# Kernel optimization log

Measured on AMD Instinct MI355X. Metric: run time of the kernel, lower is better.

Reference implementation:

```python
import jax, jax.numpy as jnp
import numpy as np

B, N, DIM, H, DH, MLP, L = 4, 1024, 1024, 16, 64, 4096, 2
C = DIM // 4  # conditioning dim = 256


def setup_inputs() -> dict:
    key = jax.random.key(0)
    ks = jax.random.split(key, 12)
    s = 0.02
    return dict(
        x=jax.random.normal(ks[0], (B, N, DIM), jnp.float32),
        mu=jax.random.normal(ks[1], (B, N, C), jnp.float32),
        f=jax.random.normal(ks[2], (B, N, C), jnp.float32),
        Wqkv=jax.random.normal(ks[3], (L, DIM, 3 * H * DH), jnp.float32) * s,
        Wout=jax.random.normal(ks[4], (L, H * DH, DIM), jnp.float32) * s,
        bout=jnp.zeros((L, DIM), jnp.float32),
        W1=jax.random.normal(ks[5], (L, DIM, MLP), jnp.float32) * s,
        b1=jnp.zeros((L, MLP), jnp.float32),
        W2=jax.random.normal(ks[6], (L, MLP, DIM), jnp.float32) * s,
        b2=jnp.zeros((L, DIM), jnp.float32),
        Wmu=jax.random.normal(ks[7], (L, C, 6 * C), jnp.float32) * s,
        bmu=jnp.zeros((L, 6 * C), jnp.float32),
        Wf=jax.random.normal(ks[8], (L, C, 6 * 3 * C), jnp.float32) * s,
        bf=jnp.zeros((L, 6 * 3 * C), jnp.float32),
        g1=jnp.ones((L, DIM), jnp.float32),
        be1=jnp.zeros((L, DIM), jnp.float32),
        g2=jnp.ones((L, DIM), jnp.float32),
        be2=jnp.zeros((L, DIM), jnp.float32),
    )


def _ln(x, g, b):
    m = jnp.mean(x, -1, keepdims=True)
    v = jnp.mean((x - m) ** 2, -1, keepdims=True)
    return (x - m) * jax.lax.rsqrt(v + 1e-5) * g + b


def reference(x, mu, f, Wqkv, Wout, bout, W1, b1, W2, b2, Wmu, bmu, Wf, bf, g1, be1, g2, be2):
    scale = DH ** -0.5
    smu = jax.nn.silu(mu)  # SiLU applied to raw conditioning, shared across layers
    sf = jax.nn.silu(f)
    for i in range(L):
        mm = smu @ Wmu[i] + bmu[i]          # [B,N,6*C]
        mf = sf @ Wf[i] + bf[i]             # [B,N,6*3*C]
        mus = jnp.split(mm, 6, axis=-1)     # each [B,N,C]
        fs = jnp.split(mf, 6, axis=-1)      # each [B,N,3C]
        sh_a, sc_a, ga_a, sh_m, sc_m, ga_m = [
            jnp.concatenate([a, b_], -1) for a, b_ in zip(mus, fs)
        ]                                   # each [B,N,DIM]
        # attention branch
        h = _ln(x, g1[i], be1[i]) * (1 + sc_a) + sh_a
        qkv = h @ Wqkv[i]                   # [B,N,3*H*DH]
        q, k, v = [t.reshape(B, N, H, DH) for t in jnp.split(qkv, 3, axis=-1)]
        att = jax.nn.softmax(jnp.einsum('bihd,bjhd->bhij', q, k) * scale, axis=-1)
        o = jnp.einsum('bhij,bjhd->bihd', att, v).reshape(B, N, H * DH)
        x = x + ga_a * (o @ Wout[i] + bout[i])
        # MLP branch
        h2 = _ln(x, g2[i], be2[i]) * (1 + sc_m) + sh_m
        mlp = jax.nn.gelu(h2 @ W1[i] + b1[i], approximate=False) @ W2[i] + b2[i]
        x = x + ga_m * mlp
    return x
```

## Files before the change

### kernel.cpp

```cpp
#include <hip/hip_runtime.h>
#include <math.h>

#define BB 4
#define NN 1024
#define DIMD 1024
#define HHN 16
#define DHH 64
#define MLPD 4096
#define LLN 2
#define CCD 256
#define BNROWS (BB*NN)

typedef __attribute__((ext_vector_type(8))) _Float16 h8;
typedef __attribute__((ext_vector_type(4))) _Float16 h4;
typedef __attribute__((ext_vector_type(4))) float f32x4;

#define GLD16(gp, lp) __builtin_amdgcn_global_load_lds( \
    (const __attribute__((address_space(1))) void*)(gp), \
    (__attribute__((address_space(3))) void*)(lp), 16, 0, 0)

__global__ __launch_bounds__(256) void silu_kernel(const float* __restrict__ in,
                                                   _Float16* __restrict__ out, int n4) {
  int i = blockIdx.x * 256 + threadIdx.x;
  if (i < n4) {
    float4 v = ((const float4*)in)[i];
    h4 o;
    o[0] = (_Float16)(v.x / (1.f + __expf(-v.x)));
    o[1] = (_Float16)(v.y / (1.f + __expf(-v.y)));
    o[2] = (_Float16)(v.z / (1.f + __expf(-v.z)));
    o[3] = (_Float16)(v.w / (1.f + __expf(-v.w)));
    ((h4*)out)[i] = o;
  }
}

__global__ __launch_bounds__(256) void transpose_cast(const float* __restrict__ in,
                                                      _Float16* __restrict__ out,
                                                      int K, int N) {
  __shared__ float tile[64][68];
  int bx = blockIdx.x * 64;
  int by = blockIdx.y * 64;
  int tid = threadIdx.x;
  int r0 = tid >> 4, c4 = (tid & 15) * 4;
  #pragma unroll
  for (int i = 0; i < 4; i++) {
    float4 v = *(const float4*)(in + (size_t)(by + r0 + i * 16) * N + bx + c4);
    *(float4*)&tile[r0 + i * 16][c4] = v;
  }
  __syncthreads();
  #pragma unroll
  for (int i = 0; i < 4; i++) {
    int orow = r0 + i * 16;
    h4 o;
    #pragma unroll
    for (int j = 0; j < 4; j++) o[j] = (_Float16)tile[c4 + j][orow];
    *(h4*)(out + (size_t)(bx + orow) * K + by + c4) = o;
  }
}

__global__ __launch_bounds__(256) void v_transpose(const _Float16* __restrict__ qkv,
                                                   _Float16* __restrict__ vt) {
  __shared__ _Float16 t[64][72];
  int n0 = blockIdx.x * 64;
  int bh = blockIdx.y;
  int b = bh >> 4;
  const _Float16* src = qkv + (size_t)b * NN * 3072 + 2048 + (bh & 15) * 64;
  int tid = threadIdx.x;
  int row = tid >> 2, c0 = (tid & 3) * 16;
  *(h8*)&t[row][c0] = *(const h8*)(src + (size_t)(n0 + row) * 3072 + c0);
  *(h8*)&t[row][c0 + 8] = *(const h8*)(src + (size_t)(n0 + row) * 3072 + c0 + 8);
  __syncthreads();
  int d = tid >> 2, ns = (tid & 3) * 16;
  h8 o0, o1;
  #pragma unroll
  for (int j = 0; j < 8; j++) { o0[j] = t[ns + j][d]; o1[j] = t[ns + 8 + j][d]; }
  _Float16* dst = vt + ((size_t)bh * 64 + d) * NN + n0 + ns;
  *(h8*)dst = o0;
  *(h8*)(dst + 8) = o1;
}

template <int EPI, int BNT>
__global__ __launch_bounds__(256) void gemm_bt(
    const _Float16* __restrict__ A, const _Float16* __restrict__ Bt,
    int M, int Nt, int K,
    const float* __restrict__ bias,
    _Float16* __restrict__ outh) {
  constexpr int NREP = BNT / 32;
  __shared__ _Float16 As[3][128 * 32];
  __shared__ _Float16 Bs[3][BNT * 32];
  const int tid = threadIdx.x;
  const int wave = tid >> 6, lane = tid & 63;
  const int brow = blockIdx.x * 128, bcol = blockIdx.y * BNT;
  const int wr = (wave >> 1) * 64, wc = (wave & 1) * (BNT / 2);
  const int r = lane & 15, g = lane >> 4;
  f32x4 acc[4][NREP];
  #pragma unroll
  for (int m = 0; m < 4; m++)
    #pragma unroll
    for (int n = 0; n < NREP; n++) acc[m][n] = (f32x4){0.f, 0.f, 0.f, 0.f};

  const int scol = ((lane & 3) ^ ((lane >> 3) & 3)) * 8;
  const _Float16* gA = A + (size_t)(brow + wave * 32 + (lane >> 2)) * K + scol;
  const _Float16* gB = Bt + (size_t)(bcol + wave * (BNT / 4) + (lane >> 2)) * K + scol;

  auto STAGE = [&](int slot, int k0) {
    GLD16(gA + k0, &As[slot][wave * 1024]);
    GLD16(gA + k0 + 16 * (size_t)K, &As[slot][wave * 1024 + 512]);
    if (BNT == 128) {
      GLD16(gB + k0, &Bs[slot][wave * 1024]);
      GLD16(gB + k0 + 16 * (size_t)K, &Bs[slot][wave * 1024 + 512]);
    } else {
      GLD16(gB + k0, &Bs[slot][wave * 512]);
    }
  };

  const int NT = K / 32;
  #pragma unroll
  for (int s = 0; s < 3; ++s)
    if (s < NT) STAGE(s, s * 32);

  const int gg = g ^ ((r >> 1) & 3);

  int cur = 0;
  for (int t = 0; t < NT; ++t) {
    const int rem = NT - 1 - t;
    if constexpr (BNT == 128) {
      if (rem >= 2)      asm volatile("s_waitcnt vmcnt(8)" ::: "memory");
      else if (rem == 1) asm volatile("s_waitcnt vmcnt(4)" ::: "memory");
      else               asm volatile("s_waitcnt vmcnt(0)" ::: "memory");
    } else {
      if (rem >= 2)      asm volatile("s_waitcnt vmcnt(6)" ::: "memory");
      else if (rem == 1) asm volatile("s_waitcnt vmcnt(3)" ::: "memory");
      else               asm volatile("s_waitcnt vmcnt(0)" ::: "memory");
    }
    __builtin_amdgcn_s_barrier();
    h8 af[4], bfr[NREP];
    #pragma unroll
    for (int m = 0; m < 4; m++) af[m] = *(const h8*)(&As[cur][(wr + m * 16 + r) * 32 + gg * 8]);
    #pragma unroll
    for (int n = 0; n < NREP; n++) bfr[n] = *(const h8*)(&Bs[cur][(wc + n * 16 + r) * 32 + gg * 8]);
    #pragma unroll
    for (int m = 0; m < 4; m++)
      #pragma unroll
      for (int n = 0; n < NREP; n++)
        acc[m][n] = __builtin_amdgcn_mfma_f32_16x16x32_f16(bfr[n], af[m], acc[m][n], 0, 0, 0);
    asm volatile("s_waitcnt lgkmcnt(0)" ::: "memory");
    __builtin_amdgcn_s_barrier();
    if (t + 3 < NT) STAGE(cur, (t + 3) * 32);
    cur = (cur == 2) ? 0 : cur + 1;
  }

  #pragma unroll
  for (int m = 0; m < 4; m++) {
    const int grow = brow + wr + m * 16 + r;
    #pragma unroll
    for (int n = 0; n < NREP; n++) {
      const int gcol = bcol + wc + n * 16 + 4 * g;
      float4 bv4 = bias ? *(const float4*)(bias + gcol) : float4{0.f, 0.f, 0.f, 0.f};
      float v[4] = {acc[m][n][0] + bv4.x, acc[m][n][1] + bv4.y,
                    acc[m][n][2] + bv4.z, acc[m][n][3] + bv4.w};
      h4 o;
      if (EPI == 0) {
        #pragma unroll
        for (int q = 0; q < 4; q++) o[q] = (_Float16)v[q];
      } else {
        #pragma unroll
        for (int q = 0; q < 4; q++)
          o[q] = (_Float16)(0.5f * v[q] * (1.f + erff(v[q] * 0.70710678118f)));
      }
      *(h4*)(outh + (size_t)grow * Nt + gcol) = o;
    }
  }
}

__global__ __launch_bounds__(256) void ln_mod_res(
    float* __restrict__ x,
    const _Float16* __restrict__ delta,
    const _Float16* __restrict__ mga, const _Float16* __restrict__ fga, int jga,
    const _Float16* __restrict__ msc, const _Float16* __restrict__ fsc, int jsh, int jsc,
    const float* __restrict__ gam, const float* __restrict__ bet,
    _Float16* __restrict__ hout) {
  const int row = blockIdx.x;
  const int tid = threadIdx.x;
  const int c0 = tid * 4;
  float* xr = x + (size_t)row * DIMD;
  float4 v = *(float4*)(xr + c0);
  if (delta) {
    h4 d4 = *(const h4*)(delta + (size_t)row * DIMD + c0);
    h4 g4 = (c0 < CCD)
        ? *(const h4*)(mga + (size_t)row * (6 * CCD) + jga * CCD + c0)
        : *(const h4*)(fga + (size_t)row * (18 * CCD) + jga * (3 * CCD) + (c0 - CCD));
    v.x += (float)g4[0] * (float)d4[0];
    v.y += (float)g4[1] * (float)d4[1];
    v.z += (float)g4[2] * (float)d4[2];
    v.w += (float)g4[3] * (float)d4[3];
    *(float4*)(xr + c0) = v;
  }
  float s = v.x + v.y + v.z + v.w;
  float sq = v.x * v.x + v.y * v.y + v.z * v.z + v.w * v.w;
  #pragma unroll
  for (int off = 32; off > 0; off >>= 1) {
    s += __shfl_down(s, off);
    sq += __shfl_down(sq, off);
  }
  __shared__ float red[8];
  int wv = tid >> 6, ln = tid & 63;
  if (ln == 0) { red[wv] = s; red[4 + wv] = sq; }
  __syncthreads();
  s = red[0] + red[1] + red[2] + red[3];
  sq = red[4] + red[5] + red[6] + red[7];
  float mean = s * (1.f / DIMD);
  float var = sq * (1.f / DIMD) - mean * mean;
  float rs = rsqrtf(var + 1e-5f);
  float4 gm = *(const float4*)(gam + c0);
  float4 bt = *(const float4*)(bet + c0);
  h4 sh4 = (c0 < CCD)
      ? *(const h4*)(msc + (size_t)row * (6 * CCD) + jsh * CCD + c0)
      : *(const h4*)(fsc + (size_t)row * (18 * CCD) + jsh * (3 * CCD) + (c0 - CCD));
  h4 sc4 = (c0 < CCD)
      ? *(const h4*)(msc + (size_t)row * (6 * CCD) + jsc * CCD + c0)
      : *(const h4*)(fsc + (size_t)row * (18 * CCD) + jsc * (3 * CCD) + (c0 - CCD));
  float xv[4] = {v.x, v.y, v.z, v.w};
  float gv[4] = {gm.x, gm.y, gm.z, gm.w};
  float bv[4] = {bt.x, bt.y, bt.z, bt.w};
  h4 o;
  #pragma unroll
  for (int i = 0; i < 4; i++) {
    float lnv = (xv[i] - mean) * rs * gv[i] + bv[i];
    o[i] = (_Float16)(lnv * (1.f + (float)sc4[i]) + (float)sh4[i]);
  }
  *((h4*)(hout + (size_t)row * DIMD + c0)) = o;
}

__global__ __launch_bounds__(256) void res_final(
    float* __restrict__ x, const _Float16* __restrict__ delta,
    const _Float16* __restrict__ mga, const _Float16* __restrict__ fga, int jga) {
  const int row = blockIdx.x;
  const int c0 = threadIdx.x * 4;
  float* xr = x + (size_t)row * DIMD;
  float4 v = *(float4*)(xr + c0);
  h4 d4 = *(const h4*)(delta + (size_t)row * DIMD + c0);
  h4 g4 = (c0 < CCD)
      ? *(const h4*)(mga + (size_t)row * (6 * CCD) + jga * CCD + c0)
      : *(const h4*)(fga + (size_t)row * (18 * CCD) + jga * (3 * CCD) + (c0 - CCD));
  v.x += (float)g4[0] * (float)d4[0];
  v.y += (float)g4[1] * (float)d4[1];
  v.z += (float)g4[2] * (float)d4[2];
  v.w += (float)g4[3] * (float)d4[3];
  *(float4*)(xr + c0) = v;
}

__global__ __launch_bounds__(256) void attn_kernel(const _Float16* __restrict__ qkv,
                                                   const _Float16* __restrict__ vt,
                                                   _Float16* __restrict__ o) {
  __shared__ _Float16 Ks[2 * 64 * 64];
  __shared__ _Float16 Vs[2 * 64 * 64];
  __shared__ _Float16 Ps[4][32 * 72];
  const int bhg = blockIdx.x * 8 + (blockIdx.y & 7);
  const int qt = blockIdx.y >> 3;
  const int b = bhg >> 4, hh = bhg & 15;
  const int tid = threadIdx.x;
  const int wave = tid >> 6, lane = tid & 63;
  const int r = lane & 15, g = lane >> 4;
  const int RS = 3 * HHN * DHH;
  const _Float16* qb = qkv + (size_t)b * NN * RS + hh * DHH;
  const _Float16* kb = qb + HHN * DHH;
  const _Float16* vtb = vt + (size_t)bhg * DHH * NN;
  const int q0 = qt * 128 + wave * 32;

  h8 qf[2][2];
  #pragma unroll
  for (int m = 0; m < 2; m++) {
    qf[m][0] = *(const h8*)(qb + (size_t)(q0 + m * 16 + r) * RS + g * 8);
    qf[m][1] = *(const h8*)(qb + (size_t)(q0 + m * 16 + r) * RS + 32 + g * 8);
  }

  f32x4 oacc[2][4];
  #pragma unroll
  for (int m = 0; m < 2; m++)
    #pragma unroll
    for (int n = 0; n < 4; n++) oacc[m][n] = (f32x4){0.f, 0.f, 0.f, 0.f};
  float mrun[2][4], lrun[2][4];
  #pragma unroll
  for (int m = 0; m < 2; m++)
    #pragma unroll
    for (int q = 0; q < 4; q++) { mrun[m][q] = -1e30f; lrun[m][q] = 0.f; }
  const float scale = 0.125f;
  _Float16* Pw = Ps[wave];

  auto STAGE = [&](int buf, int k0) {
    #pragma unroll
    for (int i = 0; i < 2; i++) {
      int chunk = wave * 2 + i;
      int blk = chunk * 64 + lane;
      int row = blk >> 3, c16 = blk & 7;
      int sc = ((c16 ^ (row & 7))) * 8;
      GLD16(kb + (size_t)(k0 + row) * RS + sc, Ks + buf * 4096 + chunk * 512);
      GLD16(vtb + (size_t)row * NN + k0 + sc, Vs + buf * 4096 + chunk * 512);
    }
  };

  STAGE(0, 0);
  int cur = 0;
  for (int kt = 0; kt < NN / 64; ++kt) {
    __syncthreads();
    if (kt + 1 < NN / 64) STAGE(cur ^ 1, (kt + 1) * 64);
    const _Float16* Kb = Ks + cur * 4096;
    const _Float16* Vb = Vs + cur * 4096;
    f32x4 sfr[2][4];
    #pragma unroll
    for (int m = 0; m < 2; m++)
      #pragma unroll
      for (int n = 0; n < 4; n++) sfr[m][n] = (f32x4){0.f, 0.f, 0.f, 0.f};
    #pragma unroll
    for (int n = 0; n < 4; n++) {
      int row = n * 16 + r, sw = row & 7;
      h8 kf0 = *(const h8*)(Kb + row * 64 + (g ^ sw) * 8);
      h8 kf1 = *(const h8*)(Kb + row * 64 + ((4 + g) ^ sw) * 8);
      #pragma unroll
      for (int m = 0; m < 2; m++) {
        sfr[m][n] = __builtin_amdgcn_mfma_f32_16x16x32_f16(qf[m][0], kf0, sfr[m][n], 0, 0, 0);
        sfr[m][n] = __builtin_amdgcn_mfma_f32_16x16x32_f16(qf[m][1], kf1, sfr[m][n], 0, 0, 0);
      }
    }
    #pragma unroll
    for (int m = 0; m < 2; m++) {
      float pm[4];
      #pragma unroll
      for (int q = 0; q < 4; q++)
        pm[q] = fmaxf(fmaxf(sfr[m][0][q], sfr[m][1][q]), fmaxf(sfr[m][2][q], sfr[m][3][q])) * scale;
      #pragma unroll
      for (int off = 1; off < 16; off <<= 1)
        #pragma unroll
        for (int q = 0; q < 4; q++) pm[q] = fmaxf(pm[q], __shfl_xor(pm[q], off));
      float fac[4], rsum[4];
      #pragma unroll
      for (int q = 0; q < 4; q++) {
        float mn = fmaxf(mrun[m][q], pm[q]);
        fac[q] = __expf(mrun[m][q] - mn);
        mrun[m][q] = mn;
        rsum[q] = 0.f;
      }
      #pragma unroll
      for (int n = 0; n < 4; n++)
        #pragma unroll
        for (int q = 0; q < 4; q++) {
          float p = __expf(sfr[m][n][q] * scale - mrun[m][q]);
          sfr[m][n][q] = p;
          rsum[q] += p;
        }
      #pragma unroll
      for (int off = 1; off < 16; off <<= 1)
        #pragma unroll
        for (int q = 0; q < 4; q++) rsum[q] += __shfl_xor(rsum[q], off);
      #pragma unroll
      for (int q = 0; q < 4; q++) lrun[m][q] = lrun[m][q] * fac[q] + rsum[q];
      #pragma unroll
      for (int n = 0; n < 4; n++)
        #pragma unroll
        for (int q = 0; q < 4; q++) oacc[m][n][q] *= fac[q];
      #pragma unroll
      for (int n = 0; n < 4; n++)
        #pragma unroll
        for (int q = 0; q < 4; q++)
          Pw[(m * 16 + 4 * g + q) * 72 + n * 16 + r] = (_Float16)sfr[m][n][q];
    }
    h8 pa[2][2];
    #pragma unroll
    for (int m = 0; m < 2; m++) {
      pa[m][0] = *(const h8*)(Pw + (m * 16 + r) * 72 + g * 8);
      pa[m][1] = *(const h8*)(Pw + (m * 16 + r) * 72 + 32 + g * 8);
    }
    #pragma unroll
    for (int nd = 0; nd < 4; nd++) {
      int row = nd * 16 + r, sw = row & 7;
      h8 vf0 = *(const h8*)(Vb + row * 64 + (g ^ sw) * 8);
      h8 vf1 = *(const h8*)(Vb + row * 64 + ((4 + g) ^ sw) * 8);
      #pragma unroll
      for (int m = 0; m < 2; m++) {
        oacc[m][nd] = __builtin_amdgcn_mfma_f32_16x16x32_f16(pa[m][0], vf0, oacc[m][nd], 0, 0, 0);
        oacc[m][nd] = __builtin_amdgcn_mfma_f32_16x16x32_f16(pa[m][1], vf1, oacc[m][nd], 0, 0, 0);
      }
    }
    cur ^= 1;
  }
  #pragma unroll
  for (int m = 0; m < 2; m++)
    #pragma unroll
    for (int nd = 0; nd < 4; nd++)
      #pragma unroll
      for (int q = 0; q < 4; q++) {
        int row = q0 + m * 16 + 4 * g + q;
        int col = hh * DHH + nd * 16 + r;
        o[((size_t)b * NN + row) * DIMD + col] = (_Float16)(oacc[m][nd][q] / lrun[m][q]);
      }
}

extern "C" void kernel_launch(void* const* d_in, const int* in_sizes, int n_in,
                              void* d_out, int out_size, void* d_ws, size_t ws_size,
                              hipStream_t stream) {
  (void)in_sizes; (void)n_in; (void)out_size; (void)ws_size;
  const float* mu   = (const float*)d_in[1];
  const float* f_in = (const float*)d_in[2];
  const float* Wqkv = (const float*)d_in[3];
  const float* Wout = (const float*)d_in[4];
  const float* bout = (const float*)d_in[5];
  const float* W1   = (const float*)d_in[6];
  const float* b1   = (const float*)d_in[7];
  const float* W2   = (const float*)d_in[8];
  const float* b2   = (const float*)d_in[9];
  const float* Wmu  = (const float*)d_in[10];
  const float* bmu  = (const float*)d_in[11];
  const float* Wf   = (const float*)d_in[12];
  const float* bfv  = (const float*)d_in[13];
  const float* g1   = (const float*)d_in[14];
  const float* be1  = (const float*)d_in[15];
  const float* g2   = (const float*)d_in[16];
  const float* be2  = (const float*)d_in[17];
  float* xout = (float*)d_out;

  char* ws = (char*)d_ws;
  size_t off = 0;
  auto alloc = [&](size_t elems) -> _Float16* {
    _Float16* p = (_Float16*)(ws + off);
    off += ((elems * 2 + 255) / 256) * 256;
    return p;
  };
  _Float16* wTqkv = alloc((size_t)LLN * 3072 * 1024);
  _Float16* wTout = alloc((size_t)LLN * 1024 * 1024);
  _Float16* wT1   = alloc((size_t)LLN * 4096 * 1024);
  _Float16* wT2   = alloc((size_t)LLN * 1024 * 4096);
  _Float16* wTmu  = alloc((size_t)LLN * 1536 * 256);
  _Float16* wTf   = alloc((size_t)LLN * 4608 * 256);
  _Float16* smu   = alloc((size_t)BNROWS * CCD);
  _Float16* sfb   = alloc((size_t)BNROWS * CCD);
  _Float16* mmb[2] = {alloc((size_t)BNROWS * 6 * CCD), alloc((size_t)BNROWS * 6 * CCD)};
  _Float16* mfb[2] = {alloc((size_t)BNROWS * 18 * CCD), alloc((size_t)BNROWS * 18 * CCD)};
  _Float16* hbuf  = alloc((size_t)BNROWS * DIMD);
  _Float16* qkvb  = alloc((size_t)BNROWS * 3 * DIMD);
  _Float16* obuf  = alloc((size_t)BNROWS * DIMD);
  _Float16* m1b   = alloc((size_t)BNROWS * MLPD);
  _Float16* vtb   = alloc((size_t)BNROWS * DIMD);
  _Float16* dres  = alloc((size_t)BNROWS * DIMD);

  hipMemcpyAsync(d_out, d_in[0], (size_t)BNROWS * DIMD * sizeof(float),
                 hipMemcpyDeviceToDevice, stream);

  silu_kernel<<<BNROWS * CCD / 4 / 256, 256, 0, stream>>>(mu, smu, BNROWS * CCD / 4);
  silu_kernel<<<BNROWS * CCD / 4 / 256, 256, 0, stream>>>(f_in, sfb, BNROWS * CCD / 4);

  for (int l = 0; l < LLN; l++) {
    transpose_cast<<<dim3(3072 / 64, 1024 / 64), 256, 0, stream>>>(
        Wqkv + (size_t)l * 1024 * 3072, wTqkv + (size_t)l * 3072 * 1024, 1024, 3072);
    transpose_cast<<<dim3(1024 / 64, 1024 / 64), 256, 0, stream>>>(
        Wout + (size_t)l * 1024 * 1024, wTout + (size_t)l * 1024 * 1024, 1024, 1024);
    transpose_cast<<<dim3(4096 / 64, 1024 / 64), 256, 0, stream>>>(
        W1 + (size_t)l * 1024 * 4096, wT1 + (size_t)l * 4096 * 1024, 1024, 4096);
    transpose_cast<<<dim3(1024 / 64, 4096 / 64), 256, 0, stream>>>(
        W2 + (size_t)l * 4096 * 1024, wT2 + (size_t)l * 1024 * 4096, 4096, 1024);
    transpose_cast<<<dim3(1536 / 64, 256 / 64), 256, 0, stream>>>(
        Wmu + (size_t)l * 256 * 1536, wTmu + (size_t)l * 1536 * 256, 256, 1536);
    transpose_cast<<<dim3(4608 / 64, 256 / 64), 256, 0, stream>>>(
        Wf + (size_t)l * 256 * 4608, wTf + (size_t)l * 4608 * 256, 256, 4608);
  }

  for (int l = 0; l < LLN; l++) {
    gemm_bt<0, 64><<<dim3(BNROWS / 128, 1536 / 64), 256, 0, stream>>>(
        smu, wTmu + (size_t)l * 1536 * 256, BNROWS, 1536, 256,
        bmu + (size_t)l * 1536, mmb[l]);
    gemm_bt<0, 128><<<dim3(BNROWS / 128, 4608 / 128), 256, 0, stream>>>(
        sfb, wTf + (size_t)l * 4608 * 256, BNROWS, 4608, 256,
        bfv + (size_t)l * 4608, mfb[l]);
    ln_mod_res<<<BNROWS, 256, 0, stream>>>(
        xout, (l == 0) ? nullptr : dres,
        mmb[l ^ 1], mfb[l ^ 1], 5,
        mmb[l], mfb[l], 0, 1,
        g1 + (size_t)l * DIMD, be1 + (size_t)l * DIMD, hbuf);
    gemm_bt<0, 128><<<dim3(BNROWS / 128, 3072 / 128), 256, 0, stream>>>(
        hbuf, wTqkv + (size_t)l * 3072 * 1024, BNROWS, 3072, 1024,
        nullptr, qkvb);
    v_transpose<<<dim3(NN / 64, BB * HHN), 256, 0, stream>>>(qkvb, vtb);
    attn_kernel<<<dim3(NN / 128, BB * HHN), 256, 0, stream>>>(qkvb, vtb, obuf);
    gemm_bt<0, 64><<<dim3(BNROWS / 128, 1024 / 64), 256, 0, stream>>>(
        obuf, wTout + (size_t)l * 1024 * 1024, BNROWS, 1024, 1024,
        bout + (size_t)l * DIMD, dres);
    ln_mod_res<<<BNROWS, 256, 0, stream>>>(
        xout, dres,
        mmb[l], mfb[l], 2,
        mmb[l], mfb[l], 3, 4,
        g2 + (size_t)l * DIMD, be2 + (size_t)l * DIMD, hbuf);
    gemm_bt<1, 128><<<dim3(BNROWS / 128, 4096 / 128), 256, 0, stream>>>(
        hbuf, wT1 + (size_t)l * 4096 * 1024, BNROWS, 4096, 1024,
        b1 + (size_t)l * MLPD, m1b);
    gemm_bt<0, 64><<<dim3(BNROWS / 128, 1024 / 64), 256, 0, stream>>>(
        m1b, wT2 + (size_t)l * 1024 * 4096, BNROWS, 1024, 4096,
        b2 + (size_t)l * DIMD, dres);
  }
  res_final<<<BNROWS, 256, 0, stream>>>(xout, dres, mmb[(LLN - 1) & 1], mfb[(LLN - 1) & 1], 5);
}
```

Before: 724.1 us.

## Split-K the N=1024 GEMMs and reduce partials in LayerNorm residual kernels

The out-projection and W2 GEMMs, which have only 1024 output columns, now use a 4-way split-K over a third grid dimension. Each split writes an fp16 partial buffer, and the downstream residual/LayerNorm kernels sum the partials and add the bias, so the grid has more blocks to fill the GPU. All GEMMs now share a 128x128 tile with a simpler double-buffered __syncthreads pipeline, replacing the triple-buffered vmcnt pipeline. The cost is extra partial-buffer traffic, fp16 rounding of each partial, and possibly weaker load/compute overlap in the large GEMMs.

```diff
diff --git a/kernel.cpp b/kernel.cpp
--- a/kernel.cpp
+++ b/kernel.cpp
@@ -10,6 +10,7 @@
 #define LLN 2
 #define CCD 256
 #define BNROWS (BB*NN)
+#define NSPLIT 4
 
 typedef __attribute__((ext_vector_type(8))) _Float16 h8;
 typedef __attribute__((ext_vector_type(4))) _Float16 h4;
@@ -78,103 +79,86 @@
   *(h8*)(dst + 8) = o1;
 }
 
-template <int EPI, int BNT>
-__global__ __launch_bounds__(256) void gemm_bt(
+template <int EPI>
+__global__ __launch_bounds__(256) void gemm128(
     const _Float16* __restrict__ A, const _Float16* __restrict__ Bt,
-    int M, int Nt, int K,
-    const float* __restrict__ bias,
-    _Float16* __restrict__ outh) {
-  constexpr int NREP = BNT / 32;
-  __shared__ _Float16 As[3][128 * 32];
-  __shared__ _Float16 Bs[3][BNT * 32];
+    int M, int Nt, int Ktot, int Kper,
+    const float* __restrict__ bias, _Float16* __restrict__ outp) {
+  __shared__ _Float16 As[2][128 * 32];
+  __shared__ _Float16 Bs[2][128 * 32];
   const int tid = threadIdx.x;
   const int wave = tid >> 6, lane = tid & 63;
-  const int brow = blockIdx.x * 128, bcol = blockIdx.y * BNT;
-  const int wr = (wave >> 1) * 64, wc = (wave & 1) * (BNT / 2);
+  const int brow = blockIdx.x * 128, bcol = blockIdx.y * 128;
+  const size_t kbase = (size_t)blockIdx.z * Kper;
+  const int wr = (wave >> 1) * 64, wc = (wave & 1) * 64;
   const int r = lane & 15, g = lane >> 4;
-  f32x4 acc[4][NREP];
+  f32x4 acc[4][4];
   #pragma unroll
   for (int m = 0; m < 4; m++)
     #pragma unroll
-    for (int n = 0; n < NREP; n++) acc[m][n] = (f32x4){0.f, 0.f, 0.f, 0.f};
+    for (int n = 0; n < 4; n++) acc[m][n] = (f32x4){0.f, 0.f, 0.f, 0.f};
 
   const int scol = ((lane & 3) ^ ((lane >> 3) & 3)) * 8;
-  const _Float16* gA = A + (size_t)(brow + wave * 32 + (lane >> 2)) * K + scol;
-  const _Float16* gB = Bt + (size_t)(bcol + wave * (BNT / 4) + (lane >> 2)) * K + scol;
+  const _Float16* gA = A + (size_t)(brow + wave * 32 + (lane >> 2)) * Ktot + kbase + scol;
+  const _Float16* gB = Bt + (size_t)(bcol + wave * 32 + (lane >> 2)) * Ktot + kbase + scol;
 
   auto STAGE = [&](int slot, int k0) {
     GLD16(gA + k0, &As[slot][wave * 1024]);
-    GLD16(gA + k0 + 16 * (size_t)K, &As[slot][wave * 1024 + 512]);
-    if (BNT == 128) {
-      GLD16(gB + k0, &Bs[slot][wave * 1024]);
-      GLD16(gB + k0 + 16 * (size_t)K, &Bs[slot][wave * 1024 + 512]);
-    } else {
-      GLD16(gB + k0, &Bs[slot][wave * 512]);
-    }
+    GLD16(gA + k0 + 16 * (size_t)Ktot, &As[slot][wave * 1024 + 512]);
+    GLD16(gB + k0, &Bs[slot][wave * 1024]);
+    GLD16(gB + k0 + 16 * (size_t)Ktot, &Bs[slot][wave * 1024 + 512]);
   };
 
-  const int NT = K / 32;
-  #pragma unroll
-  for (int s = 0; s < 3; ++s)
-    if (s < NT) STAGE(s, s * 32);
-
+  const int NT = Kper / 32;
+  STAGE(0, 0);
   const int gg = g ^ ((r >> 1) & 3);
-
   int cur = 0;
   for (int t = 0; t < NT; ++t) {
-    const int rem = NT - 1 - t;
-    if constexpr (BNT == 128) {
-      if (rem >= 2)      asm volatile("s_waitcnt vmcnt(8)" ::: "memory");
-      else if (rem == 1) asm volatile("s_waitcnt vmcnt(4)" ::: "memory");
-      else               asm volatile("s_waitcnt vmcnt(0)" ::: "memory");
-    } else {
-      if (rem >= 2)      asm volatile("s_waitcnt vmcnt(6)" ::: "memory");
-      else if (rem == 1) asm volatile("s_waitcnt vmcnt(3)" ::: "memory");
-      else               asm volatile("s_waitcnt vmcnt(0)" ::: "memory");
-    }
-    __builtin_amdgcn_s_barrier();
-    h8 af[4], bfr[NREP];
+    __syncthreads();
+    if (t + 1 < NT) STAGE(cur ^ 1, (t + 1) * 32);
+    h8 af[4], bf[4];
     #pragma unroll
     for (int m = 0; m < 4; m++) af[m] = *(const h8*)(&As[cur][(wr + m * 16 + r) * 32 + gg * 8]);
     #pragma unroll
-    for (int n = 0; n < NREP; n++) bfr[n] = *(const h8*)(&Bs[cur][(wc + n * 16 + r) * 32 + gg * 8]);
+    for (int n = 0; n < 4; n++) bf[n] = *(const h8*)(&Bs[cur][(wc + n * 16 + r) * 32 + gg * 8]);
     #pragma unroll
     for (int m = 0; m < 4; m++)
       #pragma unroll
-      for (int n = 0; n < NREP; n++)
-        acc[m][n] = __builtin_amdgcn_mfma_f32_16x16x32_f16(bfr[n], af[m], acc[m][n], 0, 0, 0);
-    asm volatile("s_waitcnt lgkmcnt(0)" ::: "memory");
-    __builtin_amdgcn_s_barrier();
-    if (t + 3 < NT) STAGE(cur, (t + 3) * 32);
-    cur = (cur == 2) ? 0 : cur + 1;
+      for (int n = 0; n < 4; n++)
+        acc[m][n] = __builtin_amdgcn_mfma_f32_16x16x32_f16(bf[n], af[m], acc[m][n], 0, 0, 0);
+    cur ^= 1;
   }
 
   #pragma unroll
   for (int m = 0; m < 4; m++) {
     const int grow = brow + wr + m * 16 + r;
     #pragma unroll
-    for (int n = 0; n < NREP; n++) {
+    for (int n = 0; n < 4; n++) {
       const int gcol = bcol + wc + n * 16 + 4 * g;
-      float4 bv4 = bias ? *(const float4*)(bias + gcol) : float4{0.f, 0.f, 0.f, 0.f};
+      float4 bv4 = (EPI != 2 && bias) ? *(const float4*)(bias + gcol)
+                                      : float4{0.f, 0.f, 0.f, 0.f};
       float v[4] = {acc[m][n][0] + bv4.x, acc[m][n][1] + bv4.y,
                     acc[m][n][2] + bv4.z, acc[m][n][3] + bv4.w};
       h4 o;
-      if (EPI == 0) {
-        #pragma unroll
-        for (int q = 0; q < 4; q++) o[q] = (_Float16)v[q];
-      } else {
+      if (EPI == 1) {
         #pragma unroll
         for (int q = 0; q < 4; q++)
           o[q] = (_Float16)(0.5f * v[q] * (1.f + erff(v[q] * 0.70710678118f)));
+      } else {
+        #pragma unroll
+        for (int q = 0; q < 4; q++) o[q] = (_Float16)v[q];
       }
-      *(h4*)(outh + (size_t)grow * Nt + gcol) = o;
+      _Float16* dst = (EPI == 2)
+          ? outp + (size_t)blockIdx.z * M * Nt + (size_t)grow * Nt + gcol
+          : outp + (size_t)grow * Nt + gcol;
+      *(h4*)dst = o;
     }
   }
 }
 
 __global__ __launch_bounds__(256) void ln_mod_res(
     float* __restrict__ x,
-    const _Float16* __restrict__ delta,
+    const _Float16* __restrict__ parts, const float* __restrict__ dbias,
     const _Float16* __restrict__ mga, const _Float16* __restrict__ fga, int jga,
     const _Float16* __restrict__ msc, const _Float16* __restrict__ fsc, int jsh, int jsc,
     const float* __restrict__ gam, const float* __restrict__ bet,
@@ -184,15 +168,22 @@
   const int c0 = tid * 4;
   float* xr = x + (size_t)row * DIMD;
   float4 v = *(float4*)(xr + c0);
-  if (delta) {
-    h4 d4 = *(const h4*)(delta + (size_t)row * DIMD + c0);
+  if (parts) {
+    float4 db = *(const float4*)(dbias + c0);
+    float d[4] = {db.x, db.y, db.z, db.w};
+    #pragma unroll
+    for (int s = 0; s < NSPLIT; s++) {
+      h4 p = *(const h4*)(parts + (size_t)s * BNROWS * DIMD + (size_t)row * DIMD + c0);
+      #pragma unroll
+      for (int i = 0; i < 4; i++) d[i] += (float)p[i];
+    }
     h4 g4 = (c0 < CCD)
         ? *(const h4*)(mga + (size_t)row * (6 * CCD) + jga * CCD + c0)
         : *(const h4*)(fga + (size_t)row * (18 * CCD) + jga * (3 * CCD) + (c0 - CCD));
-    v.x += (float)g4[0] * (float)d4[0];
-    v.y += (float)g4[1] * (float)d4[1];
-    v.z += (float)g4[2] * (float)d4[2];
-    v.w += (float)g4[3] * (float)d4[3];
+    v.x += (float)g4[0] * d[0];
+    v.y += (float)g4[1] * d[1];
+    v.z += (float)g4[2] * d[2];
+    v.w += (float)g4[3] * d[3];
     *(float4*)(xr + c0) = v;
   }
   float s = v.x + v.y + v.z + v.w;
@@ -232,20 +223,28 @@
 }
 
 __global__ __launch_bounds__(256) void res_final(
-    float* __restrict__ x, const _Float16* __restrict__ delta,
+    float* __restrict__ x,
+    const _Float16* __restrict__ parts, const float* __restrict__ dbias,
     const _Float16* __restrict__ mga, const _Float16* __restrict__ fga, int jga) {
   const int row = blockIdx.x;
   const int c0 = threadIdx.x * 4;
   float* xr = x + (size_t)row * DIMD;
   float4 v = *(float4*)(xr + c0);
-  h4 d4 = *(const h4*)(delta + (size_t)row * DIMD + c0);
+  float4 db = *(const float4*)(dbias + c0);
+  float d[4] = {db.x, db.y, db.z, db.w};
+  #pragma unroll
+  for (int s = 0; s < NSPLIT; s++) {
+    h4 p = *(const h4*)(parts + (size_t)s * BNROWS * DIMD + (size_t)row * DIMD + c0);
+    #pragma unroll
+    for (int i = 0; i < 4; i++) d[i] += (float)p[i];
+  }
   h4 g4 = (c0 < CCD)
       ? *(const h4*)(mga + (size_t)row * (6 * CCD) + jga * CCD + c0)
       : *(const h4*)(fga + (size_t)row * (18 * CCD) + jga * (3 * CCD) + (c0 - CCD));
-  v.x += (float)g4[0] * (float)d4[0];
-  v.y += (float)g4[1] * (float)d4[1];
-  v.z += (float)g4[2] * (float)d4[2];
-  v.w += (float)g4[3] * (float)d4[3];
+  v.x += (float)g4[0] * d[0];
+  v.y += (float)g4[1] * d[1];
+  v.z += (float)g4[2] * d[2];
+  v.w += (float)g4[3] * d[3];
   *(float4*)(xr + c0) = v;
 }
 
@@ -436,11 +435,12 @@
   _Float16* mmb[2] = {alloc((size_t)BNROWS * 6 * CCD), alloc((size_t)BNROWS * 6 * CCD)};
   _Float16* mfb[2] = {alloc((size_t)BNROWS * 18 * CCD), alloc((size_t)BNROWS * 18 * CCD)};
   _Float16* hbuf  = alloc((size_t)BNROWS * DIMD);
-  _Float16* qkvb  = alloc((size_t)BNROWS * 3 * DIMD);
   _Float16* obuf  = alloc((size_t)BNROWS * DIMD);
   _Float16* m1b   = alloc((size_t)BNROWS * MLPD);
-  _Float16* vtb   = alloc((size_t)BNROWS * DIMD);
-  _Float16* dres  = alloc((size_t)BNROWS * DIMD);
+  _Float16* region = alloc((size_t)NSPLIT * BNROWS * DIMD);
+  _Float16* qkvb  = region;
+  _Float16* vtb   = region + (size_t)BNROWS * 3 * DIMD;
+  _Float16* parts = region;
 
   hipMemcpyAsync(d_out, d_in[0], (size_t)BNROWS * DIMD * sizeof(float),
                  hipMemcpyDeviceToDevice, stream);
@@ -464,36 +464,38 @@
   }
 
   for (int l = 0; l < LLN; l++) {
-    gemm_bt<0, 64><<<dim3(BNROWS / 128, 1536 / 64), 256, 0, stream>>>(
-        smu, wTmu + (size_t)l * 1536 * 256, BNROWS, 1536, 256,
+    gemm128<0><<<dim3(BNROWS / 128, 1536 / 128), 256, 0, stream>>>(
+        smu, wTmu + (size_t)l * 1536 * 256, BNROWS, 1536, 256, 256,
         bmu + (size_t)l * 1536, mmb[l]);
-    gemm_bt<0, 128><<<dim3(BNROWS / 128, 4608 / 128), 256, 0, stream>>>(
-        sfb, wTf + (size_t)l * 4608 * 256, BNROWS, 4608, 256,
+    gemm128<0><<<dim3(BNROWS / 128, 4608 / 128), 256, 0, stream>>>(
+        sfb, wTf + (size_t)l * 4608 * 256, BNROWS, 4608, 256, 256,
         bfv + (size_t)l * 4608, mfb[l]);
     ln_mod_res<<<BNROWS, 256, 0, stream>>>(
-        xout, (l == 0) ? nullptr : dres,
+        xout, (l == 0) ? nullptr : parts,
+        (l == 0) ? nullptr : b2 + (size_t)(l - 1) * DIMD,
         mmb[l ^ 1], mfb[l ^ 1], 5,
         mmb[l], mfb[l], 0, 1,
         g1 + (size_t)l * DIMD, be1 + (size_t)l * DIMD, hbuf);
-    gemm_bt<0, 128><<<dim3(BNROWS / 128, 3072 / 128), 256, 0, stream>>>(
-        hbuf, wTqkv + (size_t)l * 3072 * 1024, BNROWS, 3072, 1024,
+    gemm128<0><<<dim3(BNROWS / 128, 3072 / 128), 256, 0, stream>>>(
+        hbuf, wTqkv + (size_t)l * 3072 * 1024, BNROWS, 3072, 1024, 1024,
         nullptr, qkvb);
     v_transpose<<<dim3(NN / 64, BB * HHN), 256, 0, stream>>>(qkvb, vtb);
     attn_kernel<<<dim3(NN / 128, BB * HHN), 256, 0, stream>>>(qkvb, vtb, obuf);
-    gemm_bt<0, 64><<<dim3(BNROWS / 128, 1024 / 64), 256, 0, stream>>>(
-        obuf, wTout + (size_t)l * 1024 * 1024, BNROWS, 1024, 1024,
-        bout + (size_t)l * DIMD, dres);
+    gemm128<2><<<dim3(BNROWS / 128, 1024 / 128, NSPLIT), 256, 0, stream>>>(
+        obuf, wTout + (size_t)l * 1024 * 1024, BNROWS, 1024, 1024, 1024 / NSPLIT,
+        nullptr, parts);
     ln_mod_res<<<BNROWS, 256, 0, stream>>>(
-        xout, dres,
+        xout, parts, bout + (size_t)l * DIMD,
         mmb[l], mfb[l], 2,
         mmb[l], mfb[l], 3, 4,
         g2 + (size_t)l * DIMD, be2 + (size_t)l * DIMD, hbuf);
-    gemm_bt<1, 128><<<dim3(BNROWS / 128, 4096 / 128), 256, 0, stream>>>(
-        hbuf, wT1 + (size_t)l * 4096 * 1024, BNROWS, 4096, 1024,
+    gemm128<1><<<dim3(BNROWS / 128, 4096 / 128), 256, 0, stream>>>(
+        hbuf, wT1 + (size_t)l * 4096 * 1024, BNROWS, 4096, 1024, 1024,
         b1 + (size_t)l * MLPD, m1b);
-    gemm_bt<0, 64><<<dim3(BNROWS / 128, 1024 / 64), 256, 0, stream>>>(
-        m1b, wT2 + (size_t)l * 1024 * 4096, BNROWS, 1024, 4096,
-        b2 + (size_t)l * DIMD, dres);
-  }
-  res_final<<<BNROWS, 256, 0, stream>>>(xout, dres, mmb[(LLN - 1) & 1], mfb[(LLN - 1) & 1], 5);
-}
+    gemm128<2><<<dim3(BNROWS / 128, 1024 / 128, NSPLIT), 256, 0, stream>>>(
+        m1b, wT2 + (size_t)l * 1024 * 4096, BNROWS, 1024, 4096, 4096 / NSPLIT,
+        nullptr, parts);
+  }
+  res_final<<<BNROWS, 256, 0, stream>>>(
+      xout, parts, b2 + (size_t)(LLN - 1) * DIMD, mmb[(LLN - 1) & 1], mfb[(LLN - 1) & 1], 5);
+}
```

After: 720.4 us. No clear change (-0.5%).
